# Kernel tuning notes

Hardware: AMD Instinct MI355X
Metric: run time of the kernel (lower is better)

## Reference

```python
import jax, jax.numpy as jnp
import numpy as np

B, T, C, H, MAX_LEN = 16, 512, 1024, 16, 512
D = C // H  # head_dim = 64

def setup_inputs() -> dict:
    key = jax.random.key(0)
    ks = jax.random.split(key, 10)
    s = 1.0 / np.sqrt(C)
    return {
        "x": jax.random.normal(ks[0], (B, T, C), dtype=jnp.float32),
        "Wq": jax.random.normal(ks[1], (C, C), dtype=jnp.float32) * s,
        "bq": jnp.zeros((C,), dtype=jnp.float32),
        "Wk": jax.random.normal(ks[2], (C, C), dtype=jnp.float32) * s,
        "bk": jnp.zeros((C,), dtype=jnp.float32),
        "Wv": jax.random.normal(ks[3], (C, C), dtype=jnp.float32) * s,
        "bv": jnp.zeros((C,), dtype=jnp.float32),
        "Wo": jax.random.normal(ks[4], (C, C), dtype=jnp.float32) * s,
        "bo": jnp.zeros((C,), dtype=jnp.float32),
        "rel_pos_bias": jax.random.normal(ks[5], (H, MAX_LEN, MAX_LEN), dtype=jnp.float32) * 0.02,
    }

def reference(x, Wq, bq, Wk, bk, Wv, bv, Wo, bo, rel_pos_bias):
    scale = 1.0 / jnp.sqrt(jnp.float32(D))
    # projections (torch Linear: x @ W.T + b), reshape to (B,H,T,D)
    def proj(W, b):
        return (x @ W.T + b).reshape(B, T, H, D).transpose(0, 2, 1, 3)
    q, k, v = proj(Wq, bq), proj(Wk, bk), proj(Wv, bv)
    attn = jnp.einsum('bhtd,bhsd->bhts', q, k) * scale  # (B,H,T,T)
    attn = attn + rel_pos_bias[None, :, :T, :T]
    causal = jnp.triu(jnp.ones((T, T), dtype=bool), k=1)
    attn = jnp.where(causal[None, None], -jnp.inf, attn)
    attn = jax.nn.softmax(attn, axis=-1)  # dropout p=0 (eval) -> identity
    out = jnp.einsum('bhts,bhsd->bhtd', attn, v)
    out = out.transpose(0, 2, 1, 3).reshape(B, T, C)
    return out @ Wo.T + bo
```

## Files before the change

### kernel.cpp

```cpp
#include <hip/hip_runtime.h>
#include <stdint.h>
#include <math.h>

#define DEV static __device__ __forceinline__

typedef __attribute__((ext_vector_type(8))) __bf16 bf16x8;
typedef __attribute__((ext_vector_type(4))) float f32x4;
typedef unsigned short u16;

DEV u16 f2b(float f) {
  union { float f; uint32_t u; } x; x.f = f;
  uint32_t r = x.u + 0x7fffu + ((x.u >> 16) & 1u);
  return (u16)(r >> 16);
}

DEV uint32_t pk2(float a, float b) {
  return (uint32_t)f2b(a) | ((uint32_t)f2b(b) << 16);
}

DEV float b2f_lo(uint32_t u) { return __uint_as_float(u << 16); }
DEV float b2f_hi(uint32_t u) { return __uint_as_float(u & 0xffff0000u); }

DEV void glds16(const void* g, void* l) {
  __builtin_amdgcn_global_load_lds(
      (const __attribute__((address_space(1))) void*)g,
      (__attribute__((address_space(3))) void*)l, 16, 0, 0);
}

DEV f32x4 mfma16(bf16x8 a, bf16x8 b, f32x4 c) {
  return __builtin_amdgcn_mfma_f32_16x16x32_bf16(a, b, c, 0, 0, 0);
}

#define BAR() __builtin_amdgcn_s_barrier()
#define WAIT_LGKM()                                      \
  {                                                      \
    asm volatile("s_waitcnt lgkmcnt(0)" ::: "memory");   \
    __builtin_amdgcn_sched_barrier(0);                   \
  }
#define WAIT_VM6() asm volatile("s_waitcnt vmcnt(6)" ::: "memory")
#define WAIT_VM3() asm volatile("s_waitcnt vmcnt(3)" ::: "memory")
#define WAIT_VM0() asm volatile("s_waitcnt vmcnt(0)" ::: "memory")

__global__ __launch_bounds__(256) void cvt_all(
    const float* __restrict__ x, const float* __restrict__ Wq,
    const float* __restrict__ Wk, const float* __restrict__ Wv,
    const float* __restrict__ Wo, const float* __restrict__ bias,
    u16* __restrict__ xb, u16* __restrict__ wqkv, u16* __restrict__ wo,
    u16* __restrict__ biasb) {
  size_t i = ((size_t)blockIdx.x * 256 + threadIdx.x) * 4;
  const float* s;
  u16* d;
  size_t off;
  float scale = 1.0f;
  if (i < 8388608)        { s = x;  d = xb;             off = i; }
  else if (i < 9437184)   { s = Wq; d = wqkv;           off = i - 8388608; }
  else if (i < 10485760)  { s = Wk; d = wqkv + 1048576; off = i - 9437184; }
  else if (i < 11534336)  { s = Wv; d = wqkv + 2097152; off = i - 10485760; }
  else if (i < 12582912)  { s = Wo; d = wo;             off = i - 11534336; }
  else { s = bias; d = biasb; off = i - 12582912; scale = 1.44269504f; }
  float4 v = *(const float4*)(s + off);
  ushort4 o;
  o.x = f2b(v.x * scale); o.y = f2b(v.y * scale);
  o.z = f2b(v.z * scale); o.w = f2b(v.w * scale);
  *(ushort4*)(d + off) = o;
}


DEV void stage_a(const u16* A, int m0, int kt, int kh, int wave, int srow,
                 int scol, u16 (*lsA)[2][8192]) {
  const u16* src =
      A + (size_t)(m0 + wave * 32 + srow) * 1024 + kt * 64 + kh * 32 + scol;
  glds16(src, &lsA[kt & 1][kh][wave * 1024]);
  glds16(src + (size_t)16 * 1024, &lsA[kt & 1][kh][wave * 1024 + 512]);
}

DEV void stage_b(const u16* Bw, int n0, int kt, int kh, int wave, int srow,
                 int scol, u16 (*lsB)[2][4096]) {
  glds16(Bw + (size_t)(n0 + wave * 16 + srow) * 1024 + kt * 64 + kh * 32 + scol,
         &lsB[kt & 1][kh][wave * 512]);
}

DEV void load_frags(const u16* Rbase, const u16* Cbase, int wr, int wc,
                    int c16, int swz, bf16x8 rf[4], bf16x8 cf[4]) {
#pragma unroll
  for (int i = 0; i < 4; ++i)
    rf[i] = *(const bf16x8*)&Rbase[(wr * 64 + i * 16 + c16) * 32 + swz];
#pragma unroll
  for (int i = 0; i < 4; ++i)
    cf[i] = *(const bf16x8*)&Cbase[(wc * 64 + i * 16 + c16) * 32 + swz];
}

DEV void mfma_all(bf16x8 rf[4], bf16x8 cf[4], f32x4 acc[4][4]) {
#pragma unroll
  for (int i = 0; i < 4; ++i)
#pragma unroll
    for (int j = 0; j < 4; ++j) acc[i][j] = mfma16(rf[i], cf[j], acc[i][j]);
}

#define GPH(BUF, KH, DOST, STT, STKH, VMW)                                 \
  {                                                                        \
    const u16* Rb = vblk ? &lsB[BUF][KH][0] : &lsA[BUF][KH][0];            \
    const u16* Cb = vblk ? &lsA[BUF][KH][0] : &lsB[BUF][KH][0];            \
    bf16x8 rf[4], cf[4];                                                   \
    load_frags(Rb, Cb, wr, wc, c16, swz, rf, cf);                          \
    if (DOST) {                                                            \
      stage_a(A, m0, (STT), (STKH), wave, srow, scol, lsA);                \
      stage_b(Bw, n0, (STT), (STKH), wave, srow, scol, lsB);               \
    }                                                                      \
    BAR();                                                                 \
    WAIT_LGKM();                                                           \
    __builtin_amdgcn_s_setprio(1);                                         \
    mfma_all(rf, cf, acc);                                                 \
    __builtin_amdgcn_s_setprio(0);                                         \
    VMW;                                                                   \
    BAR();                                                                 \
  }

DEV void gemm_core(const u16* A, const u16* Bw, int m0, int n0, bool vblk,
                   int wave, int lane, u16 (*lsA)[2][8192],
                   u16 (*lsB)[2][4096], f32x4 acc[4][4]) {
  int q16 = lane >> 4, c16 = lane & 15;
  int wm = wave >> 1, wn = wave & 1;
  int wr = vblk ? wn : wm, wc = vblk ? wm : wn;
  int srow = lane >> 2;
  int scol = ((lane & 3) ^ ((lane >> 3) & 3)) * 8;
  int swz = (q16 ^ ((c16 >> 1) & 3)) * 8;

  stage_a(A, m0, 0, 0, wave, srow, scol, lsA);
  stage_b(Bw, n0, 0, 0, wave, srow, scol, lsB);
  stage_a(A, m0, 0, 1, wave, srow, scol, lsA);
  stage_b(Bw, n0, 0, 1, wave, srow, scol, lsB);
  stage_a(A, m0, 1, 0, wave, srow, scol, lsA);
  stage_b(Bw, n0, 1, 0, wave, srow, scol, lsB);
  WAIT_VM6();
  BAR();

  for (int j = 0; j < 7; ++j) {
    GPH(0, 0, true, 2 * j + 1, 1, WAIT_VM6());
    GPH(0, 1, true, 2 * j + 2, 0, WAIT_VM6());
    GPH(1, 0, true, 2 * j + 2, 1, WAIT_VM6());
    GPH(1, 1, true, 2 * j + 3, 0, WAIT_VM6());
  }
  GPH(0, 0, true, 15, 1, WAIT_VM6());
  GPH(0, 1, false, 0, 0, WAIT_VM3());
  GPH(1, 0, false, 0, 0, WAIT_VM0());
  GPH(1, 1, false, 0, 0, );
}

__global__ __launch_bounds__(512, 2) void gemm_qkv(
    const u16* __restrict__ A, const u16* __restrict__ Bw,
    const float* __restrict__ bq, const float* __restrict__ bk,
    const float* __restrict__ bv,
    u16* __restrict__ qo, u16* __restrict__ ko, u16* __restrict__ vto) {
  __shared__ u16 lsA[2][2][8192];
  __shared__ u16 lsB[2][2][4096];
  int tid = threadIdx.x, wave = tid >> 6, lane = tid & 63;
  int q16 = lane >> 4, c16 = lane & 15;
  int m0 = blockIdx.y * 256, n0 = blockIdx.x * 128;
  int wm = wave >> 1, wn = wave & 1;
  const bool vblk = (n0 >= 2048);

  f32x4 acc[4][4];
#pragma unroll
  for (int i = 0; i < 4; ++i)
#pragma unroll
    for (int j = 0; j < 4; ++j) acc[i][j] = (f32x4)0.0f;

  gemm_core(A, Bw, m0, n0, vblk, wave, lane, lsA, lsB, acc);

  if (!vblk) {
#pragma unroll
    for (int mt = 0; mt < 4; ++mt) {
#pragma unroll
      for (int nt = 0; nt < 4; ++nt) {
        int n = n0 + wn * 64 + nt * 16 + c16;
        int which = n >> 10;
        int nl = n & 1023;
        int hh = nl >> 6, d = nl & 63;
        float bias = (which == 0 ? bq : bk)[nl];
        u16* dst = (which == 0 ? qo : ko);
#pragma unroll
        for (int r = 0; r < 4; ++r) {
          int m = m0 + wm * 64 + mt * 16 + q16 * 4 + r;
          int b = m >> 9, t = m & 511;
          size_t bh = (size_t)b * 16 + hh;
          dst[(bh * 512 + t) * 72 + d] = f2b(acc[mt][nt][r] + bias);
        }
      }
    }
  } else {
#pragma unroll
    for (int it = 0; it < 4; ++it) {
      int nbase = n0 + wn * 64 + it * 16 + q16 * 4;
      float4 bvv = *(const float4*)(bv + (nbase & 1023));
#pragma unroll
      for (int jt = 0; jt < 4; ++jt) {
        int m = m0 + wm * 64 + jt * 16 + c16;
        int b = m >> 9, t = m & 511;
        size_t bh4 = ((size_t)b * 16) * 4;
#pragma unroll
        for (int r = 0; r < 4; ++r) {
          int nl = (nbase + r) & 1023;
          int hh = nl >> 6, d = nl & 63;
          float bias = ((const float*)&bvv)[r];
          vto[((bh4 + (size_t)hh * 4 + (t >> 7)) * 64 + d) * 136 + (t & 127)] =
              f2b(acc[it][jt][r] + bias);
        }
      }
    }
  }
}

__global__ __launch_bounds__(256, 3) void attn_kernel(
    const u16* __restrict__ qglob, const u16* __restrict__ kglob,
    const u16* __restrict__ vtglob, const u16* __restrict__ biasb,
    u16* __restrict__ og) {
  __shared__ u16 lsK[128 * 72];
  __shared__ u16 lsV[64 * 136];
  __shared__ u16 lsP[4 * 32 * 72];

  int tid = threadIdx.x, wave = tid >> 6, lane = tid & 63;
  int q16 = lane >> 4, c16 = lane & 15;
  u16* lsPw = lsP + wave * (32 * 72);

  int p = blockIdx.x;
  int bx, bh, bx2 = -1, bh2 = 0;
  if (p < 256)      { bx = 3; bh = p; }
  else if (p < 512) { bx = 2; bh = p - 256; bx2 = 0; bh2 = p - 256; }
  else              { int q = p - 512; bx = 1; bh = 2 * q; bx2 = 1; bh2 = 2 * q + 1; }

  for (;;) {
    int b = bh >> 4, h = bh & 15;
    int q0 = bx * 128;

    const u16* qbase = qglob + (size_t)bh * (512 * 72) + (size_t)q0 * 72;
    const u16* kbase = kglob + (size_t)bh * (512 * 72);
    const u16* vbase = vtglob + (size_t)bh * 4 * (64 * 136);

    for (int i = wave; i < 18; i += 4)
      glds16(qbase + (size_t)i * 512 + lane * 8, lsK + i * 512);
    __syncthreads();
    bf16x8 qf[2][2];
#pragma unroll
    for (int nt = 0; nt < 2; ++nt)
#pragma unroll
      for (int ks = 0; ks < 2; ++ks)
        qf[nt][ks] = *(const bf16x8*)&lsK[(wave * 32 + nt * 16 + c16) * 72 +
                                          ks * 32 + q16 * 8];

    f32x4 oacc[2][4];
#pragma unroll
    for (int i = 0; i < 2; ++i)
#pragma unroll
      for (int j = 0; j < 4; ++j) oacc[i][j] = (f32x4)0.0f;
    float mold[2] = {-INFINITY, -INFINITY};
    float lsum[2] = {0.0f, 0.0f};
    const float SCL = 0.18033688f;

    for (int st = 0; st <= bx; ++st) {
      bool diag = (st == bx);
      __syncthreads();
      const u16* kt = kbase + (size_t)st * (128 * 72);
      for (int i = wave; i < 18; i += 4)
        glds16(kt + (size_t)i * 512 + lane * 8, lsK + i * 512);
      const u16* vt = vbase + (size_t)st * (64 * 136);
      for (int i = wave; i < 17; i += 4)
        glds16(vt + (size_t)i * 512 + lane * 8, lsV + i * 512);

      uint2 ub[2][8];
#pragma unroll
      for (int nt = 0; nt < 2; ++nt) {
        int qgl = q0 + wave * 32 + nt * 16 + c16;
        const u16* bp =
            biasb + ((size_t)h * 512 + qgl) * 512 + st * 128 + q16 * 4;
#pragma unroll
        for (int mt = 0; mt < 8; ++mt) ub[nt][mt] = *(const uint2*)(bp + mt * 16);
      }
      __syncthreads();

      f32x4 sa[8][2];
#pragma unroll
      for (int mt = 0; mt < 8; ++mt) {
        sa[mt][0] = (f32x4)0.0f;
        sa[mt][1] = (f32x4)0.0f;
      }
      int mtmax = diag ? 2 * wave + 2 : 8;
#pragma unroll
      for (int mt = 0; mt < 8; ++mt) {
        if (mt < mtmax) {
#pragma unroll
          for (int ks = 0; ks < 2; ++ks) {
            bf16x8 kf =
                *(const bf16x8*)&lsK[(mt * 16 + c16) * 72 + ks * 32 + q16 * 8];
            sa[mt][0] = mfma16(kf, qf[0][ks], sa[mt][0]);
            sa[mt][1] = mfma16(kf, qf[1][ks], sa[mt][1]);
          }
        }
      }

      float alpha[2];
#pragma unroll
      for (int nt = 0; nt < 2; ++nt) {
#pragma unroll
        for (int mt = 0; mt < 8; ++mt) {
          uint32_t lo = ub[nt][mt].x, hi = ub[nt][mt].y;
          f32x4 bv;
          bv[0] = b2f_lo(lo); bv[1] = b2f_hi(lo);
          bv[2] = b2f_lo(hi); bv[3] = b2f_hi(hi);
          sa[mt][nt] = sa[mt][nt] * SCL + bv;
        }
        if (diag) {
#pragma unroll
          for (int mt = 0; mt < 8; ++mt) {
            int d0 = mt * 16 + q16 * 4 - wave * 32 - nt * 16 - c16;
#pragma unroll
            for (int r = 0; r < 4; ++r)
              if (d0 + r > 0) sa[mt][nt][r] = -INFINITY;
          }
        }
        f32x4 m4 = sa[0][nt];
#pragma unroll
        for (int mt = 1; mt < 8; ++mt) {
          f32x4 v = sa[mt][nt];
          m4[0] = fmaxf(m4[0], v[0]); m4[1] = fmaxf(m4[1], v[1]);
          m4[2] = fmaxf(m4[2], v[2]); m4[3] = fmaxf(m4[3], v[3]);
        }
        float mx = fmaxf(fmaxf(m4[0], m4[1]), fmaxf(m4[2], m4[3]));
        mx = fmaxf(mx, __shfl_xor(mx, 16));
        mx = fmaxf(mx, __shfl_xor(mx, 32));
        float mnew = fmaxf(mold[nt], mx);
        alpha[nt] = exp2f(mold[nt] - mnew);
        mold[nt] = mnew;
        f32x4 s4 = (f32x4)0.0f;
#pragma unroll
        for (int mt = 0; mt < 8; ++mt) {
          f32x4 pq;
          pq[0] = exp2f(sa[mt][nt][0] - mnew);
          pq[1] = exp2f(sa[mt][nt][1] - mnew);
          pq[2] = exp2f(sa[mt][nt][2] - mnew);
          pq[3] = exp2f(sa[mt][nt][3] - mnew);
          sa[mt][nt] = pq;
          s4 += pq;
        }
        float ss = (s4[0] + s4[1]) + (s4[2] + s4[3]);
        ss += __shfl_xor(ss, 16);
        ss += __shfl_xor(ss, 32);
        lsum[nt] = lsum[nt] * alpha[nt] + ss;
      }

#pragma unroll
      for (int mo = 0; mo < 2; ++mo) {
        f32x4 av;
#pragma unroll
        for (int r = 0; r < 4; ++r) av[r] = __shfl(alpha[mo], q16 * 4 + r);
#pragma unroll
        for (int dt = 0; dt < 4; ++dt) oacc[mo][dt] *= av;
      }

      int G = diag ? wave + 1 : 4;
#pragma unroll
      for (int hf = 0; hf < 2; ++hf) {
        if (hf * 2 < G) {
#pragma unroll
          for (int nt = 0; nt < 2; ++nt)
#pragma unroll
            for (int mt4 = 0; mt4 < 4; ++mt4) {
              f32x4 pv = sa[hf * 4 + mt4][nt];
              uint2 w;
              w.x = pk2(pv[0], pv[1]);
              w.y = pk2(pv[2], pv[3]);
              *(uint2*)&lsPw[(nt * 16 + c16) * 72 + mt4 * 16 + q16 * 4] = w;
            }
#pragma unroll
          for (int ksh = 0; ksh < 2; ++ksh) {
            if (hf * 2 + ksh < G) {
              bf16x8 pf0 =
                  *(const bf16x8*)&lsPw[c16 * 72 + ksh * 32 + q16 * 8];
              bf16x8 pf1 =
                  *(const bf16x8*)&lsPw[(16 + c16) * 72 + ksh * 32 + q16 * 8];
#pragma unroll
              for (int dt = 0; dt < 4; ++dt) {
                bf16x8 vf = *(const bf16x8*)&lsV[(dt * 16 + c16) * 136 +
                                                 hf * 64 + ksh * 32 + q16 * 8];
                oacc[0][dt] = mfma16(pf0, vf, oacc[0][dt]);
                oacc[1][dt] = mfma16(pf1, vf, oacc[1][dt]);
              }
            }
          }
        }
      }
    }

#pragma unroll
    for (int mo = 0; mo < 2; ++mo) {
      f32x4 lv;
#pragma unroll
      for (int r = 0; r < 4; ++r) lv[r] = __shfl(lsum[mo], q16 * 4 + r);
#pragma unroll
      for (int r = 0; r < 4; ++r) {
        int tg = q0 + wave * 32 + mo * 16 + q16 * 4 + r;
        float inv = 1.0f / lv[r];
#pragma unroll
        for (int dt = 0; dt < 4; ++dt)
          og[((size_t)b * 512 + tg) * 1024 + h * 64 + dt * 16 + c16] =
              f2b(oacc[mo][dt][r] * inv);
      }
    }

    if (bx2 < 0) break;
    __syncthreads();
    bx = bx2; bh = bh2; bx2 = -1;
  }
}

__global__ __launch_bounds__(512, 2) void gemm_out(
    const u16* __restrict__ A, const u16* __restrict__ W,
    const float* __restrict__ bo, float* __restrict__ out) {
  __shared__ u16 lsA[2][2][8192];
  __shared__ u16 lsB[2][2][4096];
  int tid = threadIdx.x, wave = tid >> 6, lane = tid & 63;
  int q16 = lane >> 4, c16 = lane & 15;
  int m0 = blockIdx.y * 256, n0 = blockIdx.x * 128;
  int wm = wave >> 1, wn = wave & 1;

  f32x4 acc[4][4];
#pragma unroll
  for (int i = 0; i < 4; ++i)
#pragma unroll
    for (int j = 0; j < 4; ++j) acc[i][j] = (f32x4)0.0f;

  gemm_core(A, W, m0, n0, false, wave, lane, lsA, lsB, acc);

#pragma unroll
  for (int mt = 0; mt < 4; ++mt) {
#pragma unroll
    for (int nt = 0; nt < 4; ++nt) {
      int n = n0 + wn * 64 + nt * 16 + c16;
      float bias = bo[n];
#pragma unroll
      for (int r = 0; r < 4; ++r) {
        int m = m0 + wm * 64 + mt * 16 + q16 * 4 + r;
        out[(size_t)m * 1024 + n] = acc[mt][nt][r] + bias;
      }
    }
  }
}

extern "C" void kernel_launch(void* const* d_in, const int* in_sizes, int n_in,
                              void* d_out, int out_size, void* d_ws, size_t ws_size,
                              hipStream_t stream) {
  const float* x    = (const float*)d_in[0];
  const float* Wq   = (const float*)d_in[1];
  const float* bq   = (const float*)d_in[2];
  const float* Wk   = (const float*)d_in[3];
  const float* bk   = (const float*)d_in[4];
  const float* Wv   = (const float*)d_in[5];
  const float* bv   = (const float*)d_in[6];
  const float* Wo   = (const float*)d_in[7];
  const float* bo   = (const float*)d_in[8];
  const float* bias = (const float*)d_in[9];
  float* out = (float*)d_out;

  const size_t MB = 1u << 20;
  char* ws = (char*)d_ws;
  u16* xb    = (u16*)(ws);
  u16* wqkv  = (u16*)(ws + 16 * MB);
  u16* wo    = (u16*)(ws + 22 * MB);
  u16* biasb = (u16*)(ws + 24 * MB);
  u16* qb    = (u16*)(ws + 32 * MB);
  u16* kb    = (u16*)(ws + 50 * MB);
  u16* vtb   = (u16*)(ws + 68 * MB);
  u16* ab    = xb;

  cvt_all<<<16384, 256, 0, stream>>>(x, Wq, Wk, Wv, Wo, bias,
                                     xb, wqkv, wo, biasb);
  gemm_qkv<<<dim3(24, 32), 512, 0, stream>>>(xb, wqkv, bq, bk, bv, qb, kb, vtb);
  attn_kernel<<<dim3(640), 256, 0, stream>>>(qb, kb, vtb, biasb, ab);
  gemm_out<<<dim3(8, 32), 512, 0, stream>>>(ab, wo, bo, out);
}
```

Baseline: 279.3 us.

## Use three-slot LDS ring pipeline in GEMMs and raise occupancy hint

Replaces the 4-slot double-buffered LDS staging (two k-tiles by two halves) in the shared GEMM core with a 3-slot ring of 32-wide K chunks, prefetching two chunks ahead in a fully unrolled 32-step loop. This shrinks the shared-memory footprint from 96KB to 72KB per block, and launch bounds are raised from 2 to 4 blocks per CU for the QKV and output GEMMs. The aim is more resident blocks to hide latency. The cost is a shallower prefetch depth and tighter register limits, which could cause spills.

After: 269.1 us. 1.04x faster.

```diff
diff --git a/kernel.cpp b/kernel.cpp
--- a/kernel.cpp
+++ b/kernel.cpp
@@ -37,7 +37,6 @@
     asm volatile("s_waitcnt lgkmcnt(0)" ::: "memory");   \
     __builtin_amdgcn_sched_barrier(0);                   \
   }
-#define WAIT_VM6() asm volatile("s_waitcnt vmcnt(6)" ::: "memory")
 #define WAIT_VM3() asm volatile("s_waitcnt vmcnt(3)" ::: "memory")
 #define WAIT_VM0() asm volatile("s_waitcnt vmcnt(0)" ::: "memory")
 
@@ -66,18 +65,13 @@
 }
 
 
-DEV void stage_a(const u16* A, int m0, int kt, int kh, int wave, int srow,
-                 int scol, u16 (*lsA)[2][8192]) {
-  const u16* src =
-      A + (size_t)(m0 + wave * 32 + srow) * 1024 + kt * 64 + kh * 32 + scol;
-  glds16(src, &lsA[kt & 1][kh][wave * 1024]);
-  glds16(src + (size_t)16 * 1024, &lsA[kt & 1][kh][wave * 1024 + 512]);
-}
-
-DEV void stage_b(const u16* Bw, int n0, int kt, int kh, int wave, int srow,
-                 int scol, u16 (*lsB)[2][4096]) {
-  glds16(Bw + (size_t)(n0 + wave * 16 + srow) * 1024 + kt * 64 + kh * 32 + scol,
-         &lsB[kt & 1][kh][wave * 512]);
+DEV void stage_slot(const u16* A, const u16* Bw, int m0, int n0, int col,
+                    int wave, int srow, int scol, u16* slotA, u16* slotB) {
+  const u16* srcA = A + (size_t)(m0 + wave * 32 + srow) * 1024 + col + scol;
+  glds16(srcA, slotA + wave * 1024);
+  glds16(srcA + (size_t)16 * 1024, slotA + wave * 1024 + 512);
+  glds16(Bw + (size_t)(n0 + wave * 16 + srow) * 1024 + col + scol,
+         slotB + wave * 512);
 }
 
 DEV void load_frags(const u16* Rbase, const u16* Cbase, int wr, int wc,
@@ -97,28 +91,9 @@
     for (int j = 0; j < 4; ++j) acc[i][j] = mfma16(rf[i], cf[j], acc[i][j]);
 }
 
-#define GPH(BUF, KH, DOST, STT, STKH, VMW)                                 \
-  {                                                                        \
-    const u16* Rb = vblk ? &lsB[BUF][KH][0] : &lsA[BUF][KH][0];            \
-    const u16* Cb = vblk ? &lsA[BUF][KH][0] : &lsB[BUF][KH][0];            \
-    bf16x8 rf[4], cf[4];                                                   \
-    load_frags(Rb, Cb, wr, wc, c16, swz, rf, cf);                          \
-    if (DOST) {                                                            \
-      stage_a(A, m0, (STT), (STKH), wave, srow, scol, lsA);                \
-      stage_b(Bw, n0, (STT), (STKH), wave, srow, scol, lsB);               \
-    }                                                                      \
-    BAR();                                                                 \
-    WAIT_LGKM();                                                           \
-    __builtin_amdgcn_s_setprio(1);                                         \
-    mfma_all(rf, cf, acc);                                                 \
-    __builtin_amdgcn_s_setprio(0);                                         \
-    VMW;                                                                   \
-    BAR();                                                                 \
-  }
-
 DEV void gemm_core(const u16* A, const u16* Bw, int m0, int n0, bool vblk,
-                   int wave, int lane, u16 (*lsA)[2][8192],
-                   u16 (*lsB)[2][4096], f32x4 acc[4][4]) {
+                   int wave, int lane, u16 (*lsA)[8192], u16 (*lsB)[4096],
+                   f32x4 acc[4][4]) {
   int q16 = lane >> 4, c16 = lane & 15;
   int wm = wave >> 1, wn = wave & 1;
   int wr = vblk ? wn : wm, wc = vblk ? wm : wn;
@@ -126,34 +101,38 @@
   int scol = ((lane & 3) ^ ((lane >> 3) & 3)) * 8;
   int swz = (q16 ^ ((c16 >> 1) & 3)) * 8;
 
-  stage_a(A, m0, 0, 0, wave, srow, scol, lsA);
-  stage_b(Bw, n0, 0, 0, wave, srow, scol, lsB);
-  stage_a(A, m0, 0, 1, wave, srow, scol, lsA);
-  stage_b(Bw, n0, 0, 1, wave, srow, scol, lsB);
-  stage_a(A, m0, 1, 0, wave, srow, scol, lsA);
-  stage_b(Bw, n0, 1, 0, wave, srow, scol, lsB);
-  WAIT_VM6();
+  stage_slot(A, Bw, m0, n0, 0, wave, srow, scol, lsA[0], lsB[0]);
+  stage_slot(A, Bw, m0, n0, 32, wave, srow, scol, lsA[1], lsB[1]);
+  WAIT_VM3();
   BAR();
 
-  for (int j = 0; j < 7; ++j) {
-    GPH(0, 0, true, 2 * j + 1, 1, WAIT_VM6());
-    GPH(0, 1, true, 2 * j + 2, 0, WAIT_VM6());
-    GPH(1, 0, true, 2 * j + 2, 1, WAIT_VM6());
-    GPH(1, 1, true, 2 * j + 3, 0, WAIT_VM6());
+#pragma unroll
+  for (int g = 0; g < 32; ++g) {
+    const int slot = g % 3;
+    const u16* Rb = vblk ? &lsB[slot][0] : &lsA[slot][0];
+    const u16* Cb = vblk ? &lsA[slot][0] : &lsB[slot][0];
+    bf16x8 rf[4], cf[4];
+    load_frags(Rb, Cb, wr, wc, c16, swz, rf, cf);
+    if (g < 30)
+      stage_slot(A, Bw, m0, n0, (g + 2) * 32, wave, srow, scol,
+                 lsA[(g + 2) % 3], lsB[(g + 2) % 3]);
+    BAR();
+    WAIT_LGKM();
+    __builtin_amdgcn_s_setprio(1);
+    mfma_all(rf, cf, acc);
+    __builtin_amdgcn_s_setprio(0);
+    if (g < 30) { WAIT_VM3(); } else if (g == 30) { WAIT_VM0(); }
+    BAR();
   }
-  GPH(0, 0, true, 15, 1, WAIT_VM6());
-  GPH(0, 1, false, 0, 0, WAIT_VM3());
-  GPH(1, 0, false, 0, 0, WAIT_VM0());
-  GPH(1, 1, false, 0, 0, );
-}
-
-__global__ __launch_bounds__(512, 2) void gemm_qkv(
+}
+
+__global__ __launch_bounds__(512, 4) void gemm_qkv(
     const u16* __restrict__ A, const u16* __restrict__ Bw,
     const float* __restrict__ bq, const float* __restrict__ bk,
     const float* __restrict__ bv,
     u16* __restrict__ qo, u16* __restrict__ ko, u16* __restrict__ vto) {
-  __shared__ u16 lsA[2][2][8192];
-  __shared__ u16 lsB[2][2][4096];
+  __shared__ u16 lsA[3][8192];
+  __shared__ u16 lsB[3][4096];
   int tid = threadIdx.x, wave = tid >> 6, lane = tid & 63;
   int q16 = lane >> 4, c16 = lane & 15;
   int m0 = blockIdx.y * 256, n0 = blockIdx.x * 128;
@@ -413,11 +392,11 @@
   }
 }
 
-__global__ __launch_bounds__(512, 2) void gemm_out(
+__global__ __launch_bounds__(512, 4) void gemm_out(
     const u16* __restrict__ A, const u16* __restrict__ W,
     const float* __restrict__ bo, float* __restrict__ out) {
-  __shared__ u16 lsA[2][2][8192];
-  __shared__ u16 lsB[2][2][4096];
+  __shared__ u16 lsA[3][8192];
+  __shared__ u16 lsB[3][4096];
   int tid = threadIdx.x, wave = tid >> 6, lane = tid & 63;
   int q16 = lane >> 4, c16 = lane & 15;
   int m0 = blockIdx.y * 256, n0 = blockIdx.x * 128;
```
